# Optimization experiments

Measured on AMD Instinct MI355X. Metric: run time of the kernel, lower is better.

The kernel has to match this reference:

```python
import jax, jax.numpy as jnp
import numpy as np

DIM = 1024
HEADS = 8
DIM_HEAD = 64
INNER = HEADS * DIM_HEAD  # 512
N_PATCHES = 256
SCALE = DIM_HEAD ** -0.5


def setup_inputs() -> dict:
    key = jax.random.key(0)
    ks = jax.random.split(key, 6)
    s = lambda fan_in: 1.0 / np.sqrt(fan_in)
    return {
        "x": jax.random.normal(ks[0], (64, N_PATCHES, DIM), dtype=jnp.float32),
        "Wq": jax.random.normal(ks[1], (DIM, INNER), dtype=jnp.float32) * s(DIM),
        "Wkv": jax.random.normal(ks[2], (DIM, 2 * INNER), dtype=jnp.float32) * s(DIM),
        "Wout": jax.random.normal(ks[3], (INNER, DIM), dtype=jnp.float32) * s(INNER),
        "bout": jax.random.normal(ks[4], (DIM,), dtype=jnp.float32) * 0.01,
        "Wspec": jax.random.normal(ks[5], (N_PATCHES, 3 * N_PATCHES), dtype=jnp.float32) * s(N_PATCHES),
    }


def reference(x, Wq, Wkv, Wout, bout, Wspec):
    b, n, d = x.shape
    # ---- spatial: single center-query attention ----
    x_center = x[:, n // 2, :]                      # [b, d]
    q = (x_center @ Wq).reshape(b, HEADS, DIM_HEAD)  # [b, h, dh]
    kv = x @ Wkv                                     # [b, n, 2*inner]
    k, v = jnp.split(kv, 2, axis=-1)
    k = k.reshape(b, n, HEADS, DIM_HEAD).transpose(0, 2, 1, 3)  # [b, h, n, dh]
    v = v.reshape(b, n, HEADS, DIM_HEAD).transpose(0, 2, 1, 3)
    logits = jnp.einsum('bhd,bhnd->bhn', q, k) * SCALE
    attn = jax.nn.softmax(logits, axis=-1)           # [b, h, n]
    out = jnp.einsum('bhn,bhnd->bhd', attn, v).reshape(b, INNER)
    # torch expands attn over n identical rows BEFORE to_out; the rows are
    # identical, so broadcasting the projected row is the same math.
    spatial = out @ Wout + bout                      # [b, d]
    spatial_out = jnp.broadcast_to(spatial[:, None, :], (b, n, d))
    # ---- spectral: attention over transposed (feature) axis ----
    x_t = x.transpose(0, 2, 1)                       # [b, d, n]
    qkv = x_t @ Wspec                                # [b, d, 3n]
    q_s, k_s, v_s = jnp.split(qkv, 3, axis=-1)       # v_s unused (as in source)
    spec_logits = jnp.einsum('bin,bjn->bij', q_s, k_s) * SCALE  # [b, d, d]
    spec_weights = jax.nn.softmax(spec_logits, axis=-1)
    return jnp.einsum('bnd,bde->bne', spatial_out, spec_weights)
```

## Files before the change

### kernel.cpp

```cpp
#include <hip/hip_runtime.h>
#include <hip/hip_bf16.h>
#include <cstdint>

typedef _Float16 f16;
typedef _Float16 half8 __attribute__((ext_vector_type(8)));
typedef float f32x4 __attribute__((ext_vector_type(4)));

#define SCALE 0.125f

#define GLL(src, dst) __builtin_amdgcn_global_load_lds( \
    (const __attribute__((address_space(1))) unsigned int*)(src), \
    (__attribute__((address_space(3))) unsigned int*)(dst), 16, 0, 0)

__global__ __launch_bounds__(256) void prep_xf(const float* __restrict__ x, f16* __restrict__ x16,
                                               f16* __restrict__ xT) {
  __shared__ f16 tile[32][33];
  int b = blockIdx.z, nt = blockIdx.y, dt = blockIdx.x;
  int c = threadIdx.x & 31, rp = threadIdx.x >> 5;
  const float* xb = x + ((size_t)b*256 + nt*32)*1024 + dt*32;
  f16* x16b = x16 + ((size_t)b*256 + nt*32)*1024 + dt*32;
#pragma unroll
  for (int p = 0; p < 4; ++p) {
    int r = p*8 + rp;
    f16 h = (f16)xb[(size_t)r*1024 + c];
    x16b[(size_t)r*1024 + c] = h;
    tile[r][c] = h;
  }
  __syncthreads();
  f16* o = xT + ((size_t)b*1024 + dt*32)*256 + nt*32;
#pragma unroll
  for (int p = 0; p < 4; ++p) { int r = p*8 + rp; o[(size_t)r*256 + c] = tile[c][r]; }
}

__global__ __launch_bounds__(256) void prep_WkvT(const float* __restrict__ W, f16* __restrict__ Wt) {
  __shared__ float tile[32][33];
  int kt = blockIdx.x, nt = blockIdx.y;
  int c = threadIdx.x & 31, rp = threadIdx.x >> 5;
#pragma unroll
  for (int p = 0; p < 4; ++p) { int r = p*8+rp; tile[r][c] = W[(size_t)(kt*32 + r)*1024 + nt*32 + c]; }
  __syncthreads();
#pragma unroll
  for (int p = 0; p < 4; ++p) { int r = p*8+rp; Wt[(size_t)(nt*32 + r)*1024 + kt*32 + c] = (f16)tile[c][r]; }
}

__global__ __launch_bounds__(256) void prep_WspecT(const float* __restrict__ W, f16* __restrict__ Wt) {
  __shared__ float tile[32][33];
  int jt = blockIdx.x, ct = blockIdx.y;
  int c = threadIdx.x & 31, rp = threadIdx.x >> 5;
#pragma unroll
  for (int p = 0; p < 4; ++p) { int r = p*8+rp; tile[r][c] = W[(size_t)(ct*32 + r)*768 + jt*32 + c]; }
  __syncthreads();
#pragma unroll
  for (int p = 0; p < 4; ++p) { int r = p*8+rp; Wt[(size_t)(jt*32 + r)*256 + ct*32 + c] = (f16)tile[c][r]; }
}

template<int KSTEPS, int AST, int BST, int CST, bool SCALEQ>
__global__ __launch_bounds__(256) void gemm128(const f16* __restrict__ Ag, const f16* __restrict__ Bg,
                                               f16* __restrict__ Cg, size_t aB, size_t bB, size_t cB) {
  __shared__ f16 As[2][128*32];
  __shared__ f16 Bs[2][128*32];
  const f16* A = Ag + (size_t)blockIdx.z*aB;
  const f16* B = Bg + (size_t)blockIdx.z*bB;
  f16* C = Cg + (size_t)blockIdx.z*cB;
  int t = threadIdx.x, lane = t & 63, wave = t >> 6;
  int l15 = lane & 15, l4 = lane >> 4;
  int wm = wave & 1, wn = wave >> 1;
  size_t m0 = (size_t)blockIdx.x*128, n0 = (size_t)blockIdx.y*128;
  float cscale = (SCALEQ && n0 < 256) ? SCALE : 1.0f;
  f32x4 acc[4][4];
#pragma unroll
  for (int i=0;i<4;++i)
#pragma unroll
    for (int j=0;j<4;++j) acc[i][j] = (f32x4){0.f,0.f,0.f,0.f};
  int rowS[2], chS[2];
#pragma unroll
  for (int c=0;c<2;++c) {
    int slot = c*256 + t;
    rowS[c] = slot >> 2;
    chS[c]  = (slot & 3) ^ ((slot >> 3) & 3);
  }
  int pc = (l4 ^ ((l15 >> 1) & 3)) * 8;

  auto STAGE = [&](int buf, int ks) {
    int k0 = ks*32;
#pragma unroll
    for (int c=0;c<2;++c) {
      GLL(A + (m0 + rowS[c])*(size_t)AST + k0 + chS[c]*8, &As[buf][(c*256 + wave*64)*8]);
      GLL(B + (n0 + rowS[c])*(size_t)BST + k0 + chS[c]*8, &Bs[buf][(c*256 + wave*64)*8]);
    }
  };

  STAGE(0, 0);
#pragma unroll 2
  for (int ks = 0; ks < KSTEPS; ++ks) {
    int cur = ks & 1;
    if (ks + 1 < KSTEPS) {
      STAGE(cur ^ 1, ks + 1);
      asm volatile("s_waitcnt vmcnt(4)" ::: "memory");
    } else {
      asm volatile("s_waitcnt vmcnt(0)" ::: "memory");
    }
    __builtin_amdgcn_s_barrier();
    __builtin_amdgcn_sched_barrier(0);
    half8 a[4], bb[4];
    const f16* Af = &As[cur][(wm*64 + l15)*32 + pc];
    const f16* Bf = &Bs[cur][(wn*64 + l15)*32 + pc];
#pragma unroll
    for (int mi=0;mi<4;++mi) a[mi]  = *(const half8*)(Af + mi*16*32);
#pragma unroll
    for (int ni=0;ni<4;++ni) bb[ni] = *(const half8*)(Bf + ni*16*32);
    __builtin_amdgcn_s_setprio(1);
#pragma unroll
    for (int mi=0;mi<4;++mi)
#pragma unroll
      for (int ni=0;ni<4;++ni)
        acc[mi][ni] = __builtin_amdgcn_mfma_f32_16x16x32_f16(a[mi], bb[ni], acc[mi][ni], 0,0,0);
    __builtin_amdgcn_s_setprio(0);
    __builtin_amdgcn_sched_barrier(0);
    __builtin_amdgcn_s_barrier();
  }
#pragma unroll
  for (int mi=0;mi<4;++mi)
#pragma unroll
    for (int ni=0;ni<4;++ni)
#pragma unroll
      for (int j=0;j<4;++j) {
        size_t row = m0 + wm*64 + mi*16 + 4*l4 + j;
        size_t col = n0 + wn*64 + ni*16 + l15;
        C[row*CST + col] = (f16)(acc[mi][ni][j] * cscale);
      }
}

__global__ __launch_bounds__(256) void qattn(const float* __restrict__ x, const float* __restrict__ Wq,
                                             const f16* __restrict__ kv, float* __restrict__ attnout) {
  int b = blockIdx.x, h = blockIdx.y;
  int t = threadIdx.x;
  __shared__ float xc[1024];
  __shared__ float qh[64];
  __shared__ float p[256];
  __shared__ float part[4][64];
  __shared__ float redw[4];
  const float* xcg = x + ((size_t)b*256 + 128)*1024;
#pragma unroll
  for (int i = 0; i < 4; ++i) xc[t + 256*i] = xcg[t + 256*i];
  __syncthreads();
  int d = t & 63, chunk = t >> 6;
  {
    float s = 0.f;
    const float* wq = Wq + (size_t)(chunk*256)*512 + h*64 + d;
#pragma unroll 8
    for (int c = 0; c < 256; ++c) s += xc[chunk*256 + c] * wq[(size_t)c*512];
    part[chunk][d] = s;
  }
  __syncthreads();
  if (t < 64) qh[t] = part[0][t]+part[1][t]+part[2][t]+part[3][t];
  __syncthreads();
  {
    const f16* kp = kv + ((size_t)b*256 + t)*1024 + h*64;
    float acc = 0.f;
#pragma unroll
    for (int d8 = 0; d8 < 8; ++d8) {
      half8 kk = *(const half8*)(kp + d8*8);
#pragma unroll
      for (int j = 0; j < 8; ++j) acc += (float)kk[j] * qh[d8*8+j];
    }
    p[t] = acc * SCALE;
  }
  __syncthreads();
  int lane = t & 63, wid = t >> 6;
  float v = p[t];
#pragma unroll
  for (int o = 32; o >= 1; o >>= 1) v = fmaxf(v, __shfl_xor(v, o));
  if (lane == 0) redw[wid] = v;
  __syncthreads();
  float m = fmaxf(fmaxf(redw[0],redw[1]),fmaxf(redw[2],redw[3]));
  float e = __expf(p[t] - m);
  __syncthreads();
  v = e;
#pragma unroll
  for (int o = 32; o >= 1; o >>= 1) v += __shfl_xor(v, o);
  if (lane == 0) redw[wid] = v;
  __syncthreads();
  float Z = redw[0]+redw[1]+redw[2]+redw[3];
  p[t] = e / Z;
  __syncthreads();
  {
    float o = 0.f;
    const f16* vp = kv + ((size_t)b*256 + chunk*64)*1024 + 512 + h*64 + d;
#pragma unroll 8
    for (int n = 0; n < 64; ++n) o += p[chunk*64 + n] * (float)vp[(size_t)n*1024];
    part[chunk][d] = o;
  }
  __syncthreads();
  if (t < 64) attnout[(size_t)b*512 + h*64 + t] = part[0][t]+part[1][t]+part[2][t]+part[3][t];
}

__global__ __launch_bounds__(256) void spatialp(const float* __restrict__ attnout, const float* __restrict__ Wout,
                                                float* __restrict__ partial) {
  int ic = blockIdx.x, b = blockIdx.y;
  int t = threadIdx.x;
  __shared__ float ao[128];
  if (t < 128) ao[t] = attnout[(size_t)b*512 + ic*128 + t];
  __syncthreads();
  const float* W = Wout + (size_t)ic*128*1024 + t*4;
  f32x4 acc0 = (f32x4){0.f,0.f,0.f,0.f};
  f32x4 acc1 = (f32x4){0.f,0.f,0.f,0.f};
#pragma unroll 4
  for (int i = 0; i < 128; i += 2) {
    f32x4 w0 = *(const f32x4*)(W + (size_t)i*1024);
    f32x4 w1 = *(const f32x4*)(W + (size_t)(i+1)*1024);
    float a0 = ao[i], a1 = ao[i+1];
    acc0[0] += a0*w0[0]; acc0[1] += a0*w0[1]; acc0[2] += a0*w0[2]; acc0[3] += a0*w0[3];
    acc1[0] += a1*w1[0]; acc1[1] += a1*w1[1]; acc1[2] += a1*w1[2]; acc1[3] += a1*w1[3];
  }
  f32x4 acc;
#pragma unroll
  for (int j=0;j<4;++j) acc[j] = acc0[j] + acc1[j];
  *(f32x4*)(partial + ((size_t)(b*4 + ic))*1024 + t*4) = acc;
}

__global__ __launch_bounds__(256) void spatialr(const float* __restrict__ partial, const float* __restrict__ bout,
                                                float* __restrict__ spatial) {
  int b = blockIdx.x, t = threadIdx.x;
  f32x4 s = *(const f32x4*)(bout + t*4);
#pragma unroll
  for (int ic = 0; ic < 4; ++ic) {
    f32x4 p = *(const f32x4*)(partial + ((size_t)(b*4 + ic))*1024 + t*4);
#pragma unroll
    for (int j=0;j<4;++j) s[j] += p[j];
  }
  *(f32x4*)(spatial + (size_t)b*1024 + t*4) = s;
}

__global__ __launch_bounds__(1024, 4) void speck(const f16* __restrict__ qks, const float* __restrict__ spatial,
                                                 float* __restrict__ r) {
  __shared__ f16 Bs[2][1024*32];
  __shared__ f16 As[2][64*32];
  __shared__ __attribute__((aligned(16))) float sz[64*16];
  __shared__ float zfin[64];
  __shared__ float spat[64];
  int bid = blockIdx.x;
  int xcd = bid & 7, q = bid >> 3;
  int b = xcd*8 + (q >> 4);
  int iblk = q & 15;
  int t = threadIdx.x, lane = t & 63, wave = t >> 6;
  int l15 = lane & 15, l4 = lane >> 4;
  const f16* qs = qks + (size_t)b*1024*512;
  int i0 = iblk*64;
  if (t < 64) spat[t] = spatial[(size_t)b*1024 + i0 + t];

  f32x4 acc[4][4];
#pragma unroll
  for (int mi=0;mi<4;++mi)
#pragma unroll
    for (int ni=0;ni<4;++ni) acc[mi][ni] = (f32x4){0.f,0.f,0.f,0.f};
  int pc = (l4 ^ ((l15 >> 1) & 3)) * 8;

  auto STAGE = [&](int buf, int ks) {
    int k0 = ks*32;
#pragma unroll
    for (int c = 0; c < 4; ++c) {
      int slot = c*1024 + t;
      int row = slot >> 2;
      int ch = (slot & 3) ^ ((slot >> 3) & 3);
      GLL(qs + (size_t)row*512 + 256 + k0 + ch*8, &Bs[buf][(c*1024 + wave*64)*8]);
    }
    if (wave < 4) {
      int slot = wave*64 + lane;
      int row = slot >> 2;
      int ch = (slot & 3) ^ ((slot >> 3) & 3);
      GLL(qs + (size_t)(i0 + row)*512 + k0 + ch*8, &As[buf][(wave*64)*8]);
    }
  };

  STAGE(0, 0);
#pragma unroll
  for (int p = 0; p < 8; ++p) {
    int buf = p & 1;
    if (p < 7) {
      STAGE(buf ^ 1, p + 1);
      if (wave < 4) asm volatile("s_waitcnt vmcnt(5)" ::: "memory");
      else          asm volatile("s_waitcnt vmcnt(4)" ::: "memory");
    } else {
      asm volatile("s_waitcnt vmcnt(0)" ::: "memory");
    }
    __builtin_amdgcn_s_barrier();
    __builtin_amdgcn_sched_barrier(0);
    half8 a[4];
#pragma unroll
    for (int mi = 0; mi < 4; ++mi) a[mi] = *(const half8*)(&As[buf][(mi*16 + l15)*32 + pc]);
    __builtin_amdgcn_s_setprio(1);
#pragma unroll
    for (int ni = 0; ni < 4; ++ni) {
      half8 bb = *(const half8*)(&Bs[buf][(wave*64 + ni*16 + l15)*32 + pc]);
#pragma unroll
      for (int mi = 0; mi < 4; ++mi)
        acc[mi][ni] = __builtin_amdgcn_mfma_f32_16x16x32_f16(a[mi], bb, acc[mi][ni], 0,0,0);
    }
    __builtin_amdgcn_s_setprio(0);
    __builtin_amdgcn_sched_barrier(0);
    __builtin_amdgcn_s_barrier();
  }
#pragma unroll
  for (int mi=0;mi<4;++mi)
#pragma unroll
    for (int jj=0;jj<4;++jj) {
      float s = 0.f;
#pragma unroll
      for (int ni=0;ni<4;++ni) {
        float e = __expf(acc[mi][ni][jj]);
        acc[mi][ni][jj] = e;
        s += e;
      }
#pragma unroll
      for (int o=1;o<16;o<<=1) s += __shfl_xor(s, o);
      if (l15 == 0) sz[(mi*16 + 4*l4 + jj)*16 + wave] = s;
    }
  __syncthreads();
  {
    float v = sz[t];
#pragma unroll
    for (int o=1;o<16;o<<=1) v += __shfl_xor(v, o);
    if ((t & 15) == 0) zfin[t >> 4] = v;
  }
  __syncthreads();
  float f[4][4];
#pragma unroll
  for (int mi=0;mi<4;++mi)
#pragma unroll
    for (int jj=0;jj<4;++jj) {
      int row = mi*16 + 4*l4 + jj;
      f[mi][jj] = spat[row] / zfin[row];
    }
  float* rb = r + (size_t)b*1024;
#pragma unroll
  for (int ni=0;ni<4;++ni) {
    float v = 0.f;
#pragma unroll
    for (int mi=0;mi<4;++mi)
#pragma unroll
      for (int jj=0;jj<4;++jj) v += f[mi][jj]*acc[mi][ni][jj];
    v += __shfl_xor(v, 16);
    v += __shfl_xor(v, 32);
    if (l4 == 0) atomicAdd(rb + wave*64 + ni*16 + l15, v);
  }
}

__global__ __launch_bounds__(256) void bcast(const float* __restrict__ r, float* __restrict__ out) {
  size_t row = blockIdx.x;
  int b = (int)(row >> 8);
  f32x4 v = *(const f32x4*)(r + (size_t)b*1024 + threadIdx.x*4);
  *(f32x4*)(out + row*1024 + (size_t)threadIdx.x*4) = v;
}

extern "C" void kernel_launch(void* const* d_in, const int* in_sizes, int n_in,
                              void* d_out, int out_size, void* d_ws, size_t ws_size,
                              hipStream_t stream) {
  const float* x     = (const float*)d_in[0];
  const float* Wq    = (const float*)d_in[1];
  const float* Wkv   = (const float*)d_in[2];
  const float* Wout  = (const float*)d_in[3];
  const float* bout  = (const float*)d_in[4];
  const float* Wspec = (const float*)d_in[5];
  float* out = (float*)d_out;
  char* ws = (char*)d_ws;
  f16*  qks     = (f16*)(ws);
  f16*  kv      = (f16*)(ws);
  float* partial = (float*)(ws);
  f16*  x16     = (f16*)(ws + 33554432);
  f16*  xT      = (f16*)(ws + 67108864);
  f16*  WkvT    = (f16*)(ws + 100663296);
  f16*  WspecT  = (f16*)(ws + 102760448);
  float* attnout = (float*)(ws + 103022592);
  float* spatial = (float*)(ws + 103153664);
  float* rvec    = (float*)(ws + 103415808);
  (void)in_sizes; (void)n_in; (void)out_size; (void)ws_size;

  prep_xf    <<<dim3(32, 8, 64), dim3(256), 0, stream>>>(x, x16, xT);
  prep_WkvT  <<<dim3(32, 32),    dim3(256), 0, stream>>>(Wkv, WkvT);
  prep_WspecT<<<dim3(16, 8),     dim3(256), 0, stream>>>(Wspec, WspecT);
  gemm128<32,1024,1024,1024,false><<<dim3(128, 8, 1), dim3(256), 0, stream>>>(x16, WkvT, kv, 0, 0, 0);
  qattn      <<<dim3(64, 8),     dim3(256), 0, stream>>>(x, Wq, kv, attnout);
  spatialp   <<<dim3(4, 64),     dim3(256), 0, stream>>>(attnout, Wout, partial);
  spatialr   <<<dim3(64),        dim3(256), 0, stream>>>(partial, bout, spatial);
  gemm128<8,256,256,512,true><<<dim3(8, 4, 64), dim3(256), 0, stream>>>(xT, WspecT, qks,
                                                                   (size_t)1024*256, 0, (size_t)1024*512);
  hipMemsetAsync(rvec, 0, 64*1024*sizeof(float), stream);
  speck      <<<dim3(1024),      dim3(1024), 0, stream>>>(qks, spatial, rvec);
  bcast      <<<dim3(16384),     dim3(256), 0, stream>>>(rvec, out);
}
```

Measured before the change: 239.4 us.

## Reassociate spatial attention to skip full KV projection; deepen speck pipeline

Instead of projecting all tokens through Wkv (a 16384x1024x1024 GEMM), the query is first folded into Wk (u = Wk q) so logits become x·u, and the softmax-weighted token average xbar is taken before applying Wv. This turns the big KV GEMM into several small GEMV-like kernels. It also restructures speck to split the 1024-wide B tile into two 512-row halves with a 4-stage B / 3-stage A buffer ring, issuing loads three stages ahead. The price is more kernel launches, extra memsets and atomics, plus a different rounding order in fp16.

```diff
diff --git a/kernel.cpp b/kernel.cpp
--- a/kernel.cpp
+++ b/kernel.cpp
@@ -30,17 +30,6 @@
   f16* o = xT + ((size_t)b*1024 + dt*32)*256 + nt*32;
 #pragma unroll
   for (int p = 0; p < 4; ++p) { int r = p*8 + rp; o[(size_t)r*256 + c] = tile[c][r]; }
-}
-
-__global__ __launch_bounds__(256) void prep_WkvT(const float* __restrict__ W, f16* __restrict__ Wt) {
-  __shared__ float tile[32][33];
-  int kt = blockIdx.x, nt = blockIdx.y;
-  int c = threadIdx.x & 31, rp = threadIdx.x >> 5;
-#pragma unroll
-  for (int p = 0; p < 4; ++p) { int r = p*8+rp; tile[r][c] = W[(size_t)(kt*32 + r)*1024 + nt*32 + c]; }
-  __syncthreads();
-#pragma unroll
-  for (int p = 0; p < 4; ++p) { int r = p*8+rp; Wt[(size_t)(nt*32 + r)*1024 + kt*32 + c] = (f16)tile[c][r]; }
 }
 
 __global__ __launch_bounds__(256) void prep_WspecT(const float* __restrict__ W, f16* __restrict__ Wt) {
@@ -131,68 +120,152 @@
       }
 }
 
-__global__ __launch_bounds__(256) void qattn(const float* __restrict__ x, const float* __restrict__ Wq,
-                                             const f16* __restrict__ kv, float* __restrict__ attnout) {
+__global__ __launch_bounds__(256) void qk(const float* __restrict__ x, const float* __restrict__ Wq,
+                                          float* __restrict__ qbuf) {
   int b = blockIdx.x, h = blockIdx.y;
   int t = threadIdx.x;
   __shared__ float xc[1024];
-  __shared__ float qh[64];
-  __shared__ float p[256];
   __shared__ float part[4][64];
-  __shared__ float redw[4];
   const float* xcg = x + ((size_t)b*256 + 128)*1024;
 #pragma unroll
   for (int i = 0; i < 4; ++i) xc[t + 256*i] = xcg[t + 256*i];
   __syncthreads();
   int d = t & 63, chunk = t >> 6;
+  float s = 0.f;
+  const float* wq = Wq + (size_t)(chunk*256)*512 + h*64 + d;
+#pragma unroll 8
+  for (int c = 0; c < 256; ++c) s += xc[chunk*256 + c] * wq[(size_t)c*512];
+  part[chunk][d] = s;
+  __syncthreads();
+  if (t < 64) qbuf[(size_t)b*512 + h*64 + t] = part[0][t]+part[1][t]+part[2][t]+part[3][t];
+}
+
+__global__ __launch_bounds__(256) void uk(const float* __restrict__ Wkv, const float* __restrict__ qbuf,
+                                          f16* __restrict__ u16) {
+  int h = blockIdx.x, dc = blockIdx.y;
+  int t = threadIdx.x;
+  __shared__ float Wk[32][64];
+  __shared__ float qT[64][65];
   {
+    int j = t & 63, g = t >> 6;
+#pragma unroll
+    for (int rr = 0; rr < 8; ++rr) {
+      int dd = g*8 + rr;
+      Wk[dd][j] = Wkv[(size_t)(dc*32 + dd)*1024 + h*64 + j];
+    }
+#pragma unroll
+    for (int rr = 0; rr < 16; ++rr) {
+      int bb = g*16 + rr;
+      qT[j][bb] = qbuf[(size_t)bb*512 + h*64 + j];
+    }
+  }
+  __syncthreads();
+  int b = t & 63, dq = t >> 6;
+#pragma unroll
+  for (int i = 0; i < 8; ++i) {
+    int dd = dq*8 + i;
     float s = 0.f;
-    const float* wq = Wq + (size_t)(chunk*256)*512 + h*64 + d;
 #pragma unroll 8
-    for (int c = 0; c < 256; ++c) s += xc[chunk*256 + c] * wq[(size_t)c*512];
-    part[chunk][d] = s;
-  }
-  __syncthreads();
-  if (t < 64) qh[t] = part[0][t]+part[1][t]+part[2][t]+part[3][t];
+    for (int j = 0; j < 64; ++j) s += qT[j][b] * Wk[dd][j];
+    u16[((size_t)b*16 + h)*1024 + dc*32 + dd] = (f16)s;
+  }
+}
+
+__global__ __launch_bounds__(64) void lgk(const f16* __restrict__ x16, const f16* __restrict__ u16,
+                                          float* __restrict__ logitbuf) {
+  int mt = blockIdx.x, b = blockIdx.y;
+  int lane = threadIdx.x, l15 = lane & 15, l4 = lane >> 4;
+  const f16* Ap = x16 + ((size_t)b*256 + mt*16 + l15)*1024 + 8*l4;
+  const f16* Bp = u16 + ((size_t)b*16 + l15)*1024 + 8*l4;
+  f32x4 acc = (f32x4){0.f,0.f,0.f,0.f};
+#pragma unroll 8
+  for (int ks = 0; ks < 32; ++ks)
+    acc = __builtin_amdgcn_mfma_f32_16x16x32_f16(*(const half8*)(Ap + ks*32),
+                                                 *(const half8*)(Bp + ks*32), acc, 0,0,0);
+  if (l15 < 8) {
+#pragma unroll
+    for (int j = 0; j < 4; ++j)
+      logitbuf[((size_t)b*256 + mt*16 + 4*l4 + j)*8 + l15] = acc[j];
+  }
+}
+
+__global__ __launch_bounds__(256) void sm(const float* __restrict__ logitbuf, f16* __restrict__ attnW) {
+  int b = blockIdx.x, t = threadIdx.x;
+  __shared__ float eL[256][9];
+  __shared__ float Zs[8];
+  float e[8];
+  const float* lp = logitbuf + (size_t)b*256*8 + (size_t)t*8;
+#pragma unroll
+  for (int h = 0; h < 8; ++h) { e[h] = __expf(lp[h] * SCALE); eL[t][h] = e[h]; }
   __syncthreads();
   {
-    const f16* kp = kv + ((size_t)b*256 + t)*1024 + h*64;
-    float acc = 0.f;
-#pragma unroll
-    for (int d8 = 0; d8 < 8; ++d8) {
-      half8 kk = *(const half8*)(kp + d8*8);
-#pragma unroll
-      for (int j = 0; j < 8; ++j) acc += (float)kk[j] * qh[d8*8+j];
-    }
-    p[t] = acc * SCALE;
-  }
-  __syncthreads();
-  int lane = t & 63, wid = t >> 6;
-  float v = p[t];
-#pragma unroll
-  for (int o = 32; o >= 1; o >>= 1) v = fmaxf(v, __shfl_xor(v, o));
-  if (lane == 0) redw[wid] = v;
-  __syncthreads();
-  float m = fmaxf(fmaxf(redw[0],redw[1]),fmaxf(redw[2],redw[3]));
-  float e = __expf(p[t] - m);
-  __syncthreads();
-  v = e;
-#pragma unroll
-  for (int o = 32; o >= 1; o >>= 1) v += __shfl_xor(v, o);
-  if (lane == 0) redw[wid] = v;
-  __syncthreads();
-  float Z = redw[0]+redw[1]+redw[2]+redw[3];
-  p[t] = e / Z;
-  __syncthreads();
+    int h = t >> 5, i = t & 31;
+    float s = 0.f;
+#pragma unroll
+    for (int k = 0; k < 8; ++k) s += eL[i + 32*k][h];
+#pragma unroll
+    for (int o = 1; o < 32; o <<= 1) s += __shfl_xor(s, o);
+    if (i == 0) Zs[h] = s;
+  }
+  __syncthreads();
+#pragma unroll
+  for (int h = 0; h < 8; ++h) attnW[((size_t)b*16 + h)*256 + t] = (f16)(e[h] / Zs[h]);
+#pragma unroll
+  for (int h = 8; h < 16; ++h) attnW[((size_t)b*16 + h)*256 + t] = (f16)0.f;
+}
+
+__global__ __launch_bounds__(64) void xbk(const f16* __restrict__ attnW, const f16* __restrict__ xT,
+                                          f16* __restrict__ xbar) {
+  int dt = blockIdx.x, b = blockIdx.y;
+  int lane = threadIdx.x, l15 = lane & 15, l4 = lane >> 4;
+  const f16* Ap = attnW + ((size_t)b*16 + l15)*256 + 8*l4;
+  const f16* Bp = xT + ((size_t)b*1024 + dt*16 + l15)*256 + 8*l4;
+  f32x4 acc = (f32x4){0.f,0.f,0.f,0.f};
+#pragma unroll
+  for (int ks = 0; ks < 8; ++ks)
+    acc = __builtin_amdgcn_mfma_f32_16x16x32_f16(*(const half8*)(Ap + ks*32),
+                                                 *(const half8*)(Bp + ks*32), acc, 0,0,0);
+  if (l4 < 2) {
+#pragma unroll
+    for (int j = 0; j < 4; ++j)
+      xbar[((size_t)b*8 + 4*l4 + j)*1024 + dt*16 + l15] = (f16)acc[j];
+  }
+}
+
+__global__ __launch_bounds__(256) void vk(const f16* __restrict__ xbar, const float* __restrict__ Wkv,
+                                          float* __restrict__ attnout) {
+  int h = blockIdx.x, dc = blockIdx.y, bc = blockIdx.z;
+  int t = threadIdx.x;
+  __shared__ float Wv[256][64];
   {
-    float o = 0.f;
-    const f16* vp = kv + ((size_t)b*256 + chunk*64)*1024 + 512 + h*64 + d;
-#pragma unroll 8
-    for (int n = 0; n < 64; ++n) o += p[chunk*64 + n] * (float)vp[(size_t)n*1024];
-    part[chunk][d] = o;
-  }
-  __syncthreads();
-  if (t < 64) attnout[(size_t)b*512 + h*64 + t] = part[0][t]+part[1][t]+part[2][t]+part[3][t];
+    int j = t & 63, g = t >> 6;
+#pragma unroll
+    for (int rr = 0; rr < 64; ++rr) {
+      int dd = g*64 + rr;
+      Wv[dd][j] = Wkv[(size_t)(dc*256 + dd)*1024 + 512 + h*64 + j];
+    }
+  }
+  __syncthreads();
+  int j = t & 63, bq = t >> 6;
+  float s[4] = {0.f,0.f,0.f,0.f};
+  const f16* xp[4];
+#pragma unroll
+  for (int bl = 0; bl < 4; ++bl)
+    xp[bl] = xbar + ((size_t)(bc*16 + bq*4 + bl)*8 + h)*1024 + dc*256;
+  for (int d8 = 0; d8 < 32; ++d8) {
+    half8 xv[4];
+#pragma unroll
+    for (int bl = 0; bl < 4; ++bl) xv[bl] = *(const half8*)(xp[bl] + d8*8);
+#pragma unroll
+    for (int i = 0; i < 8; ++i) {
+      float w = Wv[d8*8 + i][j];
+#pragma unroll
+      for (int bl = 0; bl < 4; ++bl) s[bl] += (float)xv[bl][i] * w;
+    }
+  }
+#pragma unroll
+  for (int bl = 0; bl < 4; ++bl)
+    atomicAdd(&attnout[(size_t)(bc*16 + bq*4 + bl)*512 + h*64 + j], s[bl]);
 }
 
 __global__ __launch_bounds__(256) void spatialp(const float* __restrict__ attnout, const float* __restrict__ Wout,
@@ -234,11 +307,11 @@
 
 __global__ __launch_bounds__(1024, 4) void speck(const f16* __restrict__ qks, const float* __restrict__ spatial,
                                                  float* __restrict__ r) {
-  __shared__ f16 Bs[2][1024*32];
-  __shared__ f16 As[2][64*32];
+  __shared__ f16 Bs[4][512*32];
+  __shared__ f16 As[3][64*32];
   __shared__ __attribute__((aligned(16))) float sz[64*16];
+  __shared__ float spat[64];
   __shared__ float zfin[64];
-  __shared__ float spat[64];
   int bid = blockIdx.x;
   int xcd = bid & 7, q = bid >> 3;
   int b = xcd*8 + (q >> 4);
@@ -256,50 +329,55 @@
     for (int ni=0;ni<4;++ni) acc[mi][ni] = (f32x4){0.f,0.f,0.f,0.f};
   int pc = (l4 ^ ((l15 >> 1) & 3)) * 8;
 
-  auto STAGE = [&](int buf, int ks) {
+  auto STAGE = [&](int p) {
+    int s = p & 3, hh = p & 1, ks = p >> 1;
     int k0 = ks*32;
 #pragma unroll
-    for (int c = 0; c < 4; ++c) {
-      int slot = c*1024 + t;
-      int row = slot >> 2;
-      int ch = (slot & 3) ^ ((slot >> 3) & 3);
-      GLL(qs + (size_t)row*512 + 256 + k0 + ch*8, &Bs[buf][(c*1024 + wave*64)*8]);
-    }
-    if (wave < 4) {
-      int slot = wave*64 + lane;
-      int row = slot >> 2;
-      int ch = (slot & 3) ^ ((slot >> 3) & 3);
-      GLL(qs + (size_t)(i0 + row)*512 + k0 + ch*8, &As[buf][(wave*64)*8]);
+    for (int c = 0; c < 2; ++c) {
+      int u = c*1024 + t;
+      int row = u >> 2;
+      int ch = (u & 3) ^ ((u >> 3) & 3);
+      GLL(qs + (size_t)(hh*512 + row)*512 + 256 + k0 + ch*8, &Bs[s][(c*1024 + wave*64)*8]);
+    }
+    if (hh == 0 && wave < 4) {
+      int u = wave*64 + lane;
+      int row = u >> 2;
+      int ch = (u & 3) ^ ((u >> 3) & 3);
+      GLL(qs + (size_t)(i0 + row)*512 + k0 + ch*8, &As[ks % 3][(wave*64)*8]);
     }
   };
 
-  STAGE(0, 0);
-#pragma unroll
-  for (int p = 0; p < 8; ++p) {
-    int buf = p & 1;
-    if (p < 7) {
-      STAGE(buf ^ 1, p + 1);
+  STAGE(0); STAGE(1); STAGE(2);
+#pragma unroll
+  for (int p = 0; p < 16; ++p) {
+    if (p < 14) {
       if (wave < 4) asm volatile("s_waitcnt vmcnt(5)" ::: "memory");
       else          asm volatile("s_waitcnt vmcnt(4)" ::: "memory");
+    } else if (p == 14) {
+      asm volatile("s_waitcnt vmcnt(2)" ::: "memory");
     } else {
       asm volatile("s_waitcnt vmcnt(0)" ::: "memory");
     }
     __builtin_amdgcn_s_barrier();
     __builtin_amdgcn_sched_barrier(0);
-    half8 a[4];
-#pragma unroll
-    for (int mi = 0; mi < 4; ++mi) a[mi] = *(const half8*)(&As[buf][(mi*16 + l15)*32 + pc]);
-    __builtin_amdgcn_s_setprio(1);
-#pragma unroll
-    for (int ni = 0; ni < 4; ++ni) {
-      half8 bb = *(const half8*)(&Bs[buf][(wave*64 + ni*16 + l15)*32 + pc]);
+    if (p < 13) STAGE(p + 3);
+    {
+      int s = p & 3, hh = p & 1, sA = (p >> 1) % 3;
+      half8 a[4];
 #pragma unroll
       for (int mi = 0; mi < 4; ++mi)
-        acc[mi][ni] = __builtin_amdgcn_mfma_f32_16x16x32_f16(a[mi], bb, acc[mi][ni], 0,0,0);
-    }
-    __builtin_amdgcn_s_setprio(0);
-    __builtin_amdgcn_sched_barrier(0);
-    __builtin_amdgcn_s_barrier();
+        a[mi] = *(const half8*)(&As[sA][(mi*16 + l15)*32 + pc]);
+      __builtin_amdgcn_s_setprio(1);
+#pragma unroll
+      for (int c = 0; c < 2; ++c) {
+        half8 bb = *(const half8*)(&Bs[s][(wave*32 + c*16 + l15)*32 + pc]);
+#pragma unroll
+        for (int mi = 0; mi < 4; ++mi)
+          acc[mi][hh*2+c] = __builtin_amdgcn_mfma_f32_16x16x32_f16(a[mi], bb, acc[mi][hh*2+c], 0,0,0);
+      }
+      __builtin_amdgcn_s_setprio(0);
+      __builtin_amdgcn_sched_barrier(0);
+    }
   }
 #pragma unroll
   for (int mi=0;mi<4;++mi)
@@ -342,7 +420,7 @@
       for (int jj=0;jj<4;++jj) v += f[mi][jj]*acc[mi][ni][jj];
     v += __shfl_xor(v, 16);
     v += __shfl_xor(v, 32);
-    if (l4 == 0) atomicAdd(rb + wave*64 + ni*16 + l15, v);
+    if (l4 == 0) atomicAdd(rb + (ni>>1)*512 + wave*32 + (ni&1)*16 + l15, v);
   }
 }
 
@@ -364,23 +442,31 @@
   const float* Wspec = (const float*)d_in[5];
   float* out = (float*)d_out;
   char* ws = (char*)d_ws;
-  f16*  qks     = (f16*)(ws);
-  f16*  kv      = (f16*)(ws);
-  float* partial = (float*)(ws);
-  f16*  x16     = (f16*)(ws + 33554432);
-  f16*  xT      = (f16*)(ws + 67108864);
-  f16*  WkvT    = (f16*)(ws + 100663296);
-  f16*  WspecT  = (f16*)(ws + 102760448);
-  float* attnout = (float*)(ws + 103022592);
-  float* spatial = (float*)(ws + 103153664);
-  float* rvec    = (float*)(ws + 103415808);
+  f16*   qks      = (f16*)(ws);
+  f16*   u16pad   = (f16*)(ws);
+  float* partial  = (float*)(ws);
+  float* logitbuf = (float*)(ws + 2097152);
+  f16*   attnW    = (f16*)(ws + 2621440);
+  f16*   xbar     = (f16*)(ws + 3145728);
+  float* qbuf     = (float*)(ws + 5242880);
+  f16*   x16      = (f16*)(ws + 33554432);
+  f16*   xT       = (f16*)(ws + 67108864);
+  f16*   WspecT   = (f16*)(ws + 102760448);
+  float* attnout  = (float*)(ws + 103022592);
+  float* spatial  = (float*)(ws + 103153664);
+  float* rvec     = (float*)(ws + 103415808);
   (void)in_sizes; (void)n_in; (void)out_size; (void)ws_size;
 
   prep_xf    <<<dim3(32, 8, 64), dim3(256), 0, stream>>>(x, x16, xT);
-  prep_WkvT  <<<dim3(32, 32),    dim3(256), 0, stream>>>(Wkv, WkvT);
   prep_WspecT<<<dim3(16, 8),     dim3(256), 0, stream>>>(Wspec, WspecT);
-  gemm128<32,1024,1024,1024,false><<<dim3(128, 8, 1), dim3(256), 0, stream>>>(x16, WkvT, kv, 0, 0, 0);
-  qattn      <<<dim3(64, 8),     dim3(256), 0, stream>>>(x, Wq, kv, attnout);
+  hipMemsetAsync(u16pad, 0, 2097152, stream);
+  hipMemsetAsync(attnout, 0, 64*512*sizeof(float), stream);
+  qk         <<<dim3(64, 8),     dim3(256), 0, stream>>>(x, Wq, qbuf);
+  uk         <<<dim3(8, 32),     dim3(256), 0, stream>>>(Wkv, qbuf, u16pad);
+  lgk        <<<dim3(16, 64),    dim3(64),  0, stream>>>(x16, u16pad, logitbuf);
+  sm         <<<dim3(64),        dim3(256), 0, stream>>>(logitbuf, attnW);
+  xbk        <<<dim3(64, 64),    dim3(64),  0, stream>>>(attnW, xT, xbar);
+  vk         <<<dim3(8, 4, 4),   dim3(256), 0, stream>>>(xbar, Wkv, attnout);
   spatialp   <<<dim3(4, 64),     dim3(256), 0, stream>>>(attnout, Wout, partial);
   spatialr   <<<dim3(64),        dim3(256), 0, stream>>>(partial, bout, spatial);
   gemm128<8,256,256,512,true><<<dim3(8, 4, 64), dim3(256), 0, stream>>>(xT, WspecT, qks,
```

Result: faster. 218.7 us (-8.7%).
